# Kernel optimization log

Measured on AMD Instinct MI355X. Metric: run time of the kernel, lower is better.

The kernel has to match this reference:

```python
import jax, jax.numpy as jnp
import numpy as np

N_NODES = 100000
N_EDGES = 1600000
IN_FEAT = 256
OUT_FEAT = 128


def setup_inputs() -> dict:
    key = jax.random.key(0)
    ks = jax.random.split(key, 8)
    x = jax.random.normal(ks[0], (N_NODES, IN_FEAT), dtype=jnp.float32)
    rows0 = jnp.sort(jax.random.randint(ks[1], (N_EDGES,), 0, N_NODES, dtype=jnp.int32))
    cols0 = jax.random.randint(ks[2], (N_EDGES,), 0, N_NODES, dtype=jnp.int32)
    vals0 = jax.random.uniform(ks[3], (N_EDGES,), dtype=jnp.float32)
    rows1 = jnp.sort(jax.random.randint(ks[4], (N_EDGES,), 0, N_NODES, dtype=jnp.int32))
    cols1 = jax.random.randint(ks[5], (N_EDGES,), 0, N_NODES, dtype=jnp.int32)
    vals1 = jax.random.uniform(ks[6], (N_EDGES,), dtype=jnp.float32)
    kw0, kw1 = jax.random.split(ks[7])
    # glorot-uniform-ish scale for [IN_FEAT, OUT_FEAT]
    limit = float(np.sqrt(6.0 / (IN_FEAT + OUT_FEAT)))
    W0 = jax.random.uniform(kw0, (IN_FEAT, OUT_FEAT), minval=-limit, maxval=limit, dtype=jnp.float32)
    W1 = jax.random.uniform(kw1, (IN_FEAT, OUT_FEAT), minval=-limit, maxval=limit, dtype=jnp.float32)
    return {"x": x, "rows0": rows0, "cols0": cols0, "vals0": vals0,
            "rows1": rows1, "cols1": cols1, "vals1": vals1, "W0": W0, "W1": W1}


def _spmm(rows, cols, vals, dense, n_rows):
    # sparse [N,N] (COO) @ dense [N,D] -> [N,D]
    gathered = vals[:, None] * dense[cols]          # [E, D]
    return jax.ops.segment_sum(gathered, rows, num_segments=n_rows)


def reference(x, rows0, cols0, vals0, rows1, cols1, vals1, W0, W1):
    # GraphConvolution with dropout=0 (identity), featureless=False, no bias, relu.
    # support_i = A_i @ (x @ W_i); output = relu(sum_i support_i)
    s0 = _spmm(rows0, cols0, vals0, x @ W0, N_NODES)
    s1 = _spmm(rows1, cols1, vals1, x @ W1, N_NODES)
    return jax.nn.relu(s0 + s1)
```

## Files before the change

kernel.cpp:

```cpp
#include <hip/hip_runtime.h>
#include <hip/hip_bf16.h>
#include <stdint.h>

#define NN   100000
#define NE   1600000
#define KIN  256
#define FOUT 128

typedef __attribute__((ext_vector_type(8))) short short8;
typedef __attribute__((ext_vector_type(4))) float f32x4;
typedef __attribute__((ext_vector_type(2))) float f32x2;

static __device__ __forceinline__ unsigned short f2bf(float f) {
  unsigned int u = __float_as_uint(f);
  u += 0x7fffu + ((u >> 16) & 1u);
  return (unsigned short)(u >> 16);
}

static __device__ __forceinline__ short8 pack8(float4 u, float4 v) {
  short8 r;
  r[0] = (short)f2bf(u.x); r[1] = (short)f2bf(u.y);
  r[2] = (short)f2bf(u.z); r[3] = (short)f2bf(u.w);
  r[4] = (short)f2bf(v.x); r[5] = (short)f2bf(v.y);
  r[6] = (short)f2bf(v.z); r[7] = (short)f2bf(v.w);
  return r;
}

__global__ void convert_w(const float* __restrict__ W0, const float* __restrict__ W1,
                          unsigned short* __restrict__ wt) {
  int n = blockIdx.x;
  int k = threadIdx.x;
  int which = blockIdx.y;
  const float* W = which ? W1 : W0;
  wt[(size_t)which * (FOUT * KIN) + n * KIN + k] = f2bf(W[k * FOUT + n]);
}

__global__ __launch_bounds__(256) void build_rowptr(const int* __restrict__ rows0,
                                                    const int* __restrict__ rows1,
                                                    int* __restrict__ rp0,
                                                    int* __restrict__ rp1) {
  const int e = blockIdx.x * 256 + threadIdx.x;
  const int* rows = blockIdx.y ? rows1 : rows0;
  int* rp = blockIdx.y ? rp1 : rp0;
  int r1 = rows[e];
  int r2 = (e + 1 < NE) ? rows[e + 1] : NN;
  if (e == 0)
    for (int r = 0; r <= r1; ++r) rp[r] = 0;
  for (int r = r1 + 1; r <= r2; ++r) rp[r] = e + 1;
}

__global__ __launch_bounds__(256) void gemm_fused(const float* __restrict__ x,
                                                  const unsigned short* __restrict__ wt,
                                                  unsigned short* __restrict__ h) {
  __shared__ __align__(16) unsigned short bbuf[2][2 * 128 * 64];

  const int tid  = threadIdx.x;
  const int lane = tid & 63;
  const int wv   = tid >> 6;
  const int m    = lane & 15;
  const int quad = lane >> 4;
  const int rowbase = blockIdx.x * 128 + wv * 32;

  int r0 = rowbase + m;
  int r1 = rowbase + 16 + m;
  int r0c = r0 < NN ? r0 : NN - 1;
  int r1c = r1 < NN ? r1 : NN - 1;
  const float* ap0 = x + (size_t)r0c * KIN + quad * 8;
  const float* ap1 = x + (size_t)r1c * KIN + quad * 8;

  f32x4 acc[2][2][8];
#pragma unroll
  for (int t = 0; t < 2; ++t)
#pragma unroll
    for (int i = 0; i < 2; ++i)
#pragma unroll
      for (int n = 0; n < 8; ++n)
        acc[t][i][n] = (f32x4){0.f, 0.f, 0.f, 0.f};

  uint4 sreg[8];
#define STAGE_LOAD(ko_) do {                                                   \
    _Pragma("unroll")                                                          \
    for (int u = 0; u < 8; ++u) {                                              \
      int pid = u * 256 + tid; int tm = pid >> 10;                             \
      int c = (pid >> 3) & 127; int s = pid & 7;                               \
      sreg[u] = *(const uint4*)(wt + (size_t)tm * (FOUT * KIN) + c * KIN +     \
                                (ko_) + s * 8);                                \
    } } while (0)
#define STAGE_WRITE(buf_) do {                                                 \
    _Pragma("unroll")                                                          \
    for (int u = 0; u < 8; ++u) {                                              \
      int pid = u * 256 + tid; int tm = pid >> 10;                             \
      int c = (pid >> 3) & 127; int s = pid & 7;                               \
      *(uint4*)&bbuf[buf_][tm * 8192 + c * 64 + ((s ^ (c & 7)) * 8)] = sreg[u];\
    } } while (0)

  float4 fc[4], fn[4];
  fc[0] = *(const float4*)(ap0);     fc[1] = *(const float4*)(ap0 + 4);
  fc[2] = *(const float4*)(ap1);     fc[3] = *(const float4*)(ap1 + 4);

  STAGE_LOAD(0);
  STAGE_WRITE(0);
  __syncthreads();

#pragma unroll
  for (int ci = 0; ci < 4; ++ci) {
    if (ci < 3) STAGE_LOAD((ci + 1) * 64);
#pragma unroll
    for (int kk = 0; kk < 2; ++kk) {
      const int ki = ci * 2 + kk;
      if (ki < 7) {
        const int off = (ki + 1) * 32;
        fn[0] = *(const float4*)(ap0 + off);     fn[1] = *(const float4*)(ap0 + off + 4);
        fn[2] = *(const float4*)(ap1 + off);     fn[3] = *(const float4*)(ap1 + off + 4);
      }
      short8 a0 = pack8(fc[0], fc[1]);
      short8 a1 = pack8(fc[2], fc[3]);
      const unsigned short* bb = &bbuf[ci & 1][0];
#pragma unroll
      for (int t = 0; t < 2; ++t)
#pragma unroll
        for (int n = 0; n < 8; ++n) {
          const int col = n * 16 + m;
          short8 b = *(const short8*)(bb + t * 8192 + col * 64 +
                                      (((kk * 4 + quad) ^ (m & 7)) * 8));
          acc[t][0][n] = __builtin_amdgcn_mfma_f32_16x16x32_bf16(a0, b, acc[t][0][n], 0, 0, 0);
          acc[t][1][n] = __builtin_amdgcn_mfma_f32_16x16x32_bf16(a1, b, acc[t][1][n], 0, 0, 0);
        }
      fc[0] = fn[0]; fc[1] = fn[1]; fc[2] = fn[2]; fc[3] = fn[3];
    }
    if (ci < 3) {
      STAGE_WRITE((ci + 1) & 1);
      __syncthreads();
    }
  }
#undef STAGE_LOAD
#undef STAGE_WRITE

  unsigned short* tile = &bbuf[0][0] + wv * 4096;
#pragma unroll
  for (int t = 0; t < 2; ++t) {
#pragma unroll
    for (int i = 0; i < 2; ++i)
#pragma unroll
      for (int n = 0; n < 8; ++n)
#pragma unroll
        for (int reg = 0; reg < 4; ++reg)
          tile[(i * 16 + quad * 4 + reg) * 128 + n * 16 + m] = f2bf(acc[t][i][n][reg]);

    unsigned short* hh = h + (size_t)t * NN * FOUT;
#pragma unroll
    for (int p = 0; p < 8; ++p) {
      int row = p * 4 + quad;
      uint4 v = *(const uint4*)&tile[row * 128 + m * 8];
      int grow = rowbase + row;
      if (grow < NN)
        *(uint4*)&hh[(size_t)grow * FOUT + m * 8] = v;
    }
  }
}

static __device__ __forceinline__ void consume8(const float* __restrict__ vals, int i,
                                                const unsigned* g, float& sx, float& sy) {
#pragma unroll
  for (int u = 0; u < 8; ++u) {
    float v = vals[i + u];
    sx += v * __uint_as_float(g[u] << 16);
    sy += v * __uint_as_float(g[u] & 0xffff0000u);
  }
}

static __device__ __forceinline__ void tail_spmm(const int* __restrict__ cols,
                                                 const float* __restrict__ vals,
                                                 const unsigned short* __restrict__ hsrc,
                                                 int i, int e, int fo,
                                                 float& sx, float& sy) {
  for (; i + 4 <= e; i += 4) {
    int c0 = cols[i], c1 = cols[i + 1], c2 = cols[i + 2], c3 = cols[i + 3];
    unsigned g0 = *(const unsigned*)(hsrc + (size_t)c0 * FOUT + fo);
    unsigned g1 = *(const unsigned*)(hsrc + (size_t)c1 * FOUT + fo);
    unsigned g2 = *(const unsigned*)(hsrc + (size_t)c2 * FOUT + fo);
    unsigned g3 = *(const unsigned*)(hsrc + (size_t)c3 * FOUT + fo);
    float v0 = vals[i], v1 = vals[i + 1], v2 = vals[i + 2], v3 = vals[i + 3];
    sx += v0 * __uint_as_float(g0 << 16);
    sy += v0 * __uint_as_float(g0 & 0xffff0000u);
    sx += v1 * __uint_as_float(g1 << 16);
    sy += v1 * __uint_as_float(g1 & 0xffff0000u);
    sx += v2 * __uint_as_float(g2 << 16);
    sy += v2 * __uint_as_float(g2 & 0xffff0000u);
    sx += v3 * __uint_as_float(g3 << 16);
    sy += v3 * __uint_as_float(g3 & 0xffff0000u);
  }
  for (; i < e; ++i) {
    int c = cols[i];
    float v = vals[i];
    unsigned g = *(const unsigned*)(hsrc + (size_t)c * FOUT + fo);
    sx += v * __uint_as_float(g << 16);
    sy += v * __uint_as_float(g & 0xffff0000u);
  }
}

__global__ __launch_bounds__(256) void spmm_relu(
    const int* __restrict__ rp0, const int* __restrict__ cols0, const float* __restrict__ vals0,
    const int* __restrict__ rp1, const int* __restrict__ cols1, const float* __restrict__ vals1,
    const unsigned short* __restrict__ h, float* __restrict__ out) {
  const int lane = threadIdx.x & 63;
  int r = blockIdx.x * 4 + (threadIdx.x >> 6);
  r = __builtin_amdgcn_readfirstlane(r);
  const int fo = lane * 2;

  const unsigned short* h0 = h;
  const unsigned short* h1 = h + (size_t)NN * FOUT;

  int i0 = __builtin_amdgcn_readfirstlane(rp0[r]);
  int e0 = __builtin_amdgcn_readfirstlane(rp0[r + 1]);
  int i1 = __builtin_amdgcn_readfirstlane(rp1[r]);
  int e1 = __builtin_amdgcn_readfirstlane(rp1[r + 1]);

  float sx = 0.f, sy = 0.f;

  while (i0 + 8 <= e0 && i1 + 8 <= e1) {
    unsigned g0[8], g1[8];
#pragma unroll
    for (int u = 0; u < 8; ++u) {
      int c = cols0[i0 + u];
      g0[u] = *(const unsigned*)(h0 + (size_t)c * FOUT + fo);
    }
#pragma unroll
    for (int u = 0; u < 8; ++u) {
      int c = cols1[i1 + u];
      g1[u] = *(const unsigned*)(h1 + (size_t)c * FOUT + fo);
    }
    consume8(vals0, i0, g0, sx, sy);
    consume8(vals1, i1, g1, sx, sy);
    i0 += 8;
    i1 += 8;
  }
  tail_spmm(cols0, vals0, h0, i0, e0, fo, sx, sy);
  tail_spmm(cols1, vals1, h1, i1, e1, fo, sx, sy);

  f32x2 o;
  o.x = sx > 0.f ? sx : 0.f;
  o.y = sy > 0.f ? sy : 0.f;
  __builtin_nontemporal_store(o, (f32x2*)(out + (size_t)r * FOUT + fo));
}

extern "C" void kernel_launch(void* const* d_in, const int* in_sizes, int n_in,
                              void* d_out, int out_size, void* d_ws, size_t ws_size,
                              hipStream_t stream) {
  const float* x     = (const float*)d_in[0];
  const int*   rows0 = (const int*)d_in[1];
  const int*   cols0 = (const int*)d_in[2];
  const float* vals0 = (const float*)d_in[3];
  const int*   rows1 = (const int*)d_in[4];
  const int*   cols1 = (const int*)d_in[5];
  const float* vals1 = (const float*)d_in[6];
  const float* W0    = (const float*)d_in[7];
  const float* W1    = (const float*)d_in[8];
  float* out = (float*)d_out;

  char* ws = (char*)d_ws;
  unsigned short* wt = (unsigned short*)(ws);
  unsigned short* h  = (unsigned short*)(ws + 131072);
  int* rp0 = (int*)(ws + 51331072);
  int* rp1 = (int*)(ws + 51731136);

  build_rowptr<<<dim3(6250, 2), 256, 0, stream>>>(rows0, rows1, rp0, rp1);
  convert_w<<<dim3(128, 2), 256, 0, stream>>>(W0, W1, wt);
  gemm_fused<<<dim3((NN + 127) / 128, 1), 256, 0, stream>>>(x, wt, h);
  spmm_relu<<<25000, 256, 0, stream>>>(rp0, cols0, vals0, rp1, cols1, vals1, h, out);
}
```

Before: 350.2 us.

## Sort row column indices in-wave and use persistent grid-stride SpMM

Each wave loads a row's column indices and values into lanes once (coalesced), sorts them with a 64-wide bitonic network so gathers hit h in ascending address order, and then broadcasts each index with readlane instead of issuing a scalar load per edge. The SpMM launch changes from one wave per row to a persistent grid of 2048 blocks that stride over rows, with launch bounds raised for occupancy. The sort adds 21 shuffle stages per row per matrix. Since the columns are uniformly random, sorting gives little locality, so the sort cost may outweigh any gain.

```diff
diff --git a/kernel.cpp b/kernel.cpp
--- a/kernel.cpp
+++ b/kernel.cpp
@@ -159,13 +159,47 @@
   }
 }
 
-static __device__ __forceinline__ void consume8(const float* __restrict__ vals, int i,
-                                                const unsigned* g, float& sx, float& sy) {
-#pragma unroll
-  for (int u = 0; u < 8; ++u) {
-    float v = vals[i + u];
-    sx += v * __uint_as_float(g[u] << 16);
-    sy += v * __uint_as_float(g[u] & 0xffff0000u);
+static __device__ __forceinline__ void bitonic64(int lane, int& c, unsigned& v) {
+#pragma unroll
+  for (int k = 2; k <= 64; k <<= 1) {
+#pragma unroll
+    for (int j = k >> 1; j > 0; j >>= 1) {
+      int oc = __shfl_xor(c, j, 64);
+      int ov = __shfl_xor((int)v, j, 64);
+      bool keepmin = ((lane & k) == 0) == ((lane & j) == 0);
+      bool take = keepmin ? (oc < c) : (oc > c);
+      if (take) { c = oc; v = (unsigned)ov; }
+    }
+  }
+}
+
+static __device__ __forceinline__ float rl_f(unsigned v, int idx) {
+  return __uint_as_float((unsigned)__builtin_amdgcn_readlane((int)v, idx));
+}
+
+static __device__ __forceinline__ void tail_sorted(int cs, unsigned vs, int p, int d,
+                                                   const unsigned short* __restrict__ hsrc,
+                                                   int fo, float& sx, float& sy) {
+  for (; p + 4 <= d; p += 4) {
+    unsigned g[4];
+#pragma unroll
+    for (int u = 0; u < 4; ++u) {
+      int c = __builtin_amdgcn_readlane(cs, p + u);
+      g[u] = *(const unsigned*)(hsrc + (size_t)c * FOUT + fo);
+    }
+#pragma unroll
+    for (int u = 0; u < 4; ++u) {
+      float v = rl_f(vs, p + u);
+      sx += v * __uint_as_float(g[u] << 16);
+      sy += v * __uint_as_float(g[u] & 0xffff0000u);
+    }
+  }
+  for (; p < d; ++p) {
+    int c = __builtin_amdgcn_readlane(cs, p);
+    float v = rl_f(vs, p);
+    unsigned g = *(const unsigned*)(hsrc + (size_t)c * FOUT + fo);
+    sx += v * __uint_as_float(g << 16);
+    sy += v * __uint_as_float(g & 0xffff0000u);
   }
 }
 
@@ -174,22 +208,6 @@
                                                  const unsigned short* __restrict__ hsrc,
                                                  int i, int e, int fo,
                                                  float& sx, float& sy) {
-  for (; i + 4 <= e; i += 4) {
-    int c0 = cols[i], c1 = cols[i + 1], c2 = cols[i + 2], c3 = cols[i + 3];
-    unsigned g0 = *(const unsigned*)(hsrc + (size_t)c0 * FOUT + fo);
-    unsigned g1 = *(const unsigned*)(hsrc + (size_t)c1 * FOUT + fo);
-    unsigned g2 = *(const unsigned*)(hsrc + (size_t)c2 * FOUT + fo);
-    unsigned g3 = *(const unsigned*)(hsrc + (size_t)c3 * FOUT + fo);
-    float v0 = vals[i], v1 = vals[i + 1], v2 = vals[i + 2], v3 = vals[i + 3];
-    sx += v0 * __uint_as_float(g0 << 16);
-    sy += v0 * __uint_as_float(g0 & 0xffff0000u);
-    sx += v1 * __uint_as_float(g1 << 16);
-    sy += v1 * __uint_as_float(g1 & 0xffff0000u);
-    sx += v2 * __uint_as_float(g2 << 16);
-    sy += v2 * __uint_as_float(g2 & 0xffff0000u);
-    sx += v3 * __uint_as_float(g3 << 16);
-    sy += v3 * __uint_as_float(g3 & 0xffff0000u);
-  }
   for (; i < e; ++i) {
     int c = cols[i];
     float v = vals[i];
@@ -199,49 +217,82 @@
   }
 }
 
-__global__ __launch_bounds__(256) void spmm_relu(
+__global__ __launch_bounds__(256, 8) void spmm_relu(
     const int* __restrict__ rp0, const int* __restrict__ cols0, const float* __restrict__ vals0,
     const int* __restrict__ rp1, const int* __restrict__ cols1, const float* __restrict__ vals1,
     const unsigned short* __restrict__ h, float* __restrict__ out) {
   const int lane = threadIdx.x & 63;
-  int r = blockIdx.x * 4 + (threadIdx.x >> 6);
-  r = __builtin_amdgcn_readfirstlane(r);
+  const int wgid = blockIdx.x * 4 + (threadIdx.x >> 6);
   const int fo = lane * 2;
 
   const unsigned short* h0 = h;
   const unsigned short* h1 = h + (size_t)NN * FOUT;
 
-  int i0 = __builtin_amdgcn_readfirstlane(rp0[r]);
-  int e0 = __builtin_amdgcn_readfirstlane(rp0[r + 1]);
-  int i1 = __builtin_amdgcn_readfirstlane(rp1[r]);
-  int e1 = __builtin_amdgcn_readfirstlane(rp1[r + 1]);
-
-  float sx = 0.f, sy = 0.f;
-
-  while (i0 + 8 <= e0 && i1 + 8 <= e1) {
-    unsigned g0[8], g1[8];
-#pragma unroll
-    for (int u = 0; u < 8; ++u) {
-      int c = cols0[i0 + u];
-      g0[u] = *(const unsigned*)(h0 + (size_t)c * FOUT + fo);
-    }
-#pragma unroll
-    for (int u = 0; u < 8; ++u) {
-      int c = cols1[i1 + u];
-      g1[u] = *(const unsigned*)(h1 + (size_t)c * FOUT + fo);
-    }
-    consume8(vals0, i0, g0, sx, sy);
-    consume8(vals1, i1, g1, sx, sy);
-    i0 += 8;
-    i1 += 8;
-  }
-  tail_spmm(cols0, vals0, h0, i0, e0, fo, sx, sy);
-  tail_spmm(cols1, vals1, h1, i1, e1, fo, sx, sy);
-
-  f32x2 o;
-  o.x = sx > 0.f ? sx : 0.f;
-  o.y = sy > 0.f ? sy : 0.f;
-  __builtin_nontemporal_store(o, (f32x2*)(out + (size_t)r * FOUT + fo));
+  for (int rr = wgid; rr < NN; rr += 8192) {
+    const int r = __builtin_amdgcn_readfirstlane(rr);
+
+    int i0 = __builtin_amdgcn_readfirstlane(rp0[r]);
+    int e0 = __builtin_amdgcn_readfirstlane(rp0[r + 1]);
+    int i1 = __builtin_amdgcn_readfirstlane(rp1[r]);
+    int e1 = __builtin_amdgcn_readfirstlane(rp1[r + 1]);
+    const int d0 = e0 - i0, d1 = e1 - i1;
+
+    float sx = 0.f, sy = 0.f;
+
+    if (d0 <= 64 && d1 <= 64) {
+      int c0s = 0x7fffffff, c1s = 0x7fffffff;
+      unsigned vb0 = 0, vb1 = 0;
+      if (lane < d0) {
+        c0s = cols0[i0 + lane];
+        vb0 = __float_as_uint(vals0[i0 + lane]);
+      }
+      if (lane < d1) {
+        c1s = cols1[i1 + lane];
+        vb1 = __float_as_uint(vals1[i1 + lane]);
+      }
+      bitonic64(lane, c0s, vb0);
+      bitonic64(lane, c1s, vb1);
+
+      int p0 = 0, p1 = 0;
+      while (p0 + 8 <= d0 && p1 + 8 <= d1) {
+        unsigned g0[8], g1[8];
+#pragma unroll
+        for (int u = 0; u < 8; ++u) {
+          int c = __builtin_amdgcn_readlane(c0s, p0 + u);
+          g0[u] = *(const unsigned*)(h0 + (size_t)c * FOUT + fo);
+        }
+#pragma unroll
+        for (int u = 0; u < 8; ++u) {
+          int c = __builtin_amdgcn_readlane(c1s, p1 + u);
+          g1[u] = *(const unsigned*)(h1 + (size_t)c * FOUT + fo);
+        }
+#pragma unroll
+        for (int u = 0; u < 8; ++u) {
+          float v = rl_f(vb0, p0 + u);
+          sx += v * __uint_as_float(g0[u] << 16);
+          sy += v * __uint_as_float(g0[u] & 0xffff0000u);
+        }
+#pragma unroll
+        for (int u = 0; u < 8; ++u) {
+          float v = rl_f(vb1, p1 + u);
+          sx += v * __uint_as_float(g1[u] << 16);
+          sy += v * __uint_as_float(g1[u] & 0xffff0000u);
+        }
+        p0 += 8;
+        p1 += 8;
+      }
+      tail_sorted(c0s, vb0, p0, d0, h0, fo, sx, sy);
+      tail_sorted(c1s, vb1, p1, d1, h1, fo, sx, sy);
+    } else {
+      tail_spmm(cols0, vals0, h0, i0, e0, fo, sx, sy);
+      tail_spmm(cols1, vals1, h1, i1, e1, fo, sx, sy);
+    }
+
+    f32x2 o;
+    o.x = sx > 0.f ? sx : 0.f;
+    o.y = sy > 0.f ? sy : 0.f;
+    __builtin_nontemporal_store(o, (f32x2*)(out + (size_t)r * FOUT + fo));
+  }
 }
 
 extern "C" void kernel_launch(void* const* d_in, const int* in_sizes, int n_in,
@@ -267,5 +318,5 @@
   build_rowptr<<<dim3(6250, 2), 256, 0, stream>>>(rows0, rows1, rp0, rp1);
   convert_w<<<dim3(128, 2), 256, 0, stream>>>(W0, W1, wt);
   gemm_fused<<<dim3((NN + 127) / 128, 1), 256, 0, stream>>>(x, wt, h);
-  spmm_relu<<<25000, 256, 0, stream>>>(rp0, cols0, vals0, rp1, cols1, vals1, h, out);
-}
+  spmm_relu<<<2048, 256, 0, stream>>>(rp0, cols0, vals0, rp1, cols1, vals1, h, out);
+}
```

Result: slower. 362.4 us (+3.5%).
